# Optimization experiments

Hardware: AMD Instinct MI355X
Metric: run time of the kernel (lower is better)

Reference implementation:

```python
import jax, jax.numpy as jnp
import numpy as np

B, L, D, H, HD = 4, 2048, 1024, 16, 64
SCALE = 1.0 / np.sqrt(HD)
NEG_INF = -1e9


def _apply_rope(x, rope):
    # x: (B, H, L, HD), rope: (L, HD)
    sin = rope[:, ::2]   # (L, HD/2)
    cos = rope[:, 1::2]  # (L, HD/2)
    x_even = x[..., ::2]
    x_odd = x[..., 1::2]
    r_even = x_even * cos - x_odd * sin
    r_odd = x_even * sin + x_odd * cos
    # interleave even/odd back: stack on new last axis then flatten
    return jnp.stack([r_even, r_odd], axis=-1).reshape(x.shape)


def setup_inputs() -> dict:
    key = jax.random.key(0)
    ks = jax.random.split(key, 10)
    s = 0.02
    inp = {
        "q_in": jax.random.normal(ks[0], (B, L, D), jnp.float32),
        "k_in": jax.random.normal(ks[1], (B, L, D), jnp.float32),
        "v_in": jax.random.normal(ks[2], (B, L, D), jnp.float32),
        "mask": jnp.broadcast_to(jnp.tril(jnp.ones((L, L), bool)), (B, L, L)),
        "rope": jax.random.normal(ks[3], (L, HD), jnp.float32),
        "Wq": jax.random.normal(ks[4], (D, H * HD), jnp.float32) * s,
        "bq": jnp.zeros((H * HD,), jnp.float32),
        "Wkv": jax.random.normal(ks[5], (D, 2 * H * HD), jnp.float32) * s,
        "bkv": jnp.zeros((2 * H * HD,), jnp.float32),
        "Wp": jax.random.normal(ks[6], (H * HD, D), jnp.float32) * s,
        "bp": jnp.zeros((D,), jnp.float32),
    }
    return inp


def reference(q_in, k_in, v_in, mask, rope, Wq, bq, Wkv, bkv, Wp, bp):
    q = q_in @ Wq + bq                       # (B, Lq, H*HD)
    kv = k_in @ Wkv + bkv                    # (B, Lk, 2*H*HD)
    k, v = jnp.split(kv, 2, axis=-1)
    q = q.reshape(B, L, H, HD).transpose(0, 2, 1, 3)  # (B, H, Lq, HD)
    k = k.reshape(B, L, H, HD).transpose(0, 2, 1, 3)
    v = v.reshape(B, L, H, HD).transpose(0, 2, 1, 3)
    # rope.shape[0] == Lq == Lk, so both branches fire
    q = _apply_rope(q, rope)
    k = _apply_rope(k, rope)
    logits = jnp.einsum("bhqd,bhkd->bhqk", q, k) * SCALE
    logits = jnp.where(mask[:, None, :, :], logits, NEG_INF)
    attn = jax.nn.softmax(logits, axis=-1)
    out = jnp.einsum("bhqk,bhkd->bhqd", attn, v)
    out = out.transpose(0, 2, 1, 3).reshape(B, L, H * HD)
    return out @ Wp + bp
```

## Files before the change

### kernel.cpp

```cpp
#include <hip/hip_runtime.h>
#include <hip/hip_bf16.h>

typedef __hip_bfloat16 bf16;
typedef short s16x8 __attribute__((ext_vector_type(8)));
typedef float f32x4 __attribute__((ext_vector_type(4)));

#define MFMA16(a, b, c) __builtin_amdgcn_mfma_f32_16x16x32_bf16(a, b, c, 0, 0, 0)
#define SCALE 0.125f

typedef __attribute__((address_space(1))) void gvoid;
typedef __attribute__((address_space(3))) void lvoid;

static __device__ __forceinline__ void lds_cp16(const bf16* g, bf16* l) {
    __builtin_amdgcn_global_load_lds((gvoid*)g, (lvoid*)l, 16, 0, 0);
}

__global__ void cast8_f32(const float* __restrict__ src, bf16* __restrict__ dst,
                          int n) {
    int i = (blockIdx.x * 256 + threadIdx.x) * 8;
    if (i >= n) return;
    float4 a = *(const float4*)(src + i);
    float4 b = *(const float4*)(src + i + 4);
    bf16 o[8];
    o[0] = __float2bfloat16(a.x); o[1] = __float2bfloat16(a.y);
    o[2] = __float2bfloat16(a.z); o[3] = __float2bfloat16(a.w);
    o[4] = __float2bfloat16(b.x); o[5] = __float2bfloat16(b.y);
    o[6] = __float2bfloat16(b.z); o[7] = __float2bfloat16(b.w);
    *(uint4*)(dst + i) = *(const uint4*)o;
}

__global__ void cast8_f32_dual(const float* __restrict__ s0,
                               bf16* __restrict__ d0,
                               const float* __restrict__ s1,
                               bf16* __restrict__ d1, int n) {
    int i = (blockIdx.x * 256 + threadIdx.x) * 8;
    const float* src;
    bf16* dst;
    if (i < n) {
        src = s0; dst = d0;
    } else {
        src = s1; dst = d1; i -= n;
    }
    float4 a = *(const float4*)(src + i);
    float4 b = *(const float4*)(src + i + 4);
    bf16 o[8];
    o[0] = __float2bfloat16(a.x); o[1] = __float2bfloat16(a.y);
    o[2] = __float2bfloat16(a.z); o[3] = __float2bfloat16(a.w);
    o[4] = __float2bfloat16(b.x); o[5] = __float2bfloat16(b.y);
    o[6] = __float2bfloat16(b.z); o[7] = __float2bfloat16(b.w);
    *(uint4*)(dst + i) = *(const uint4*)o;
}

__global__ void cast_biases(const float* __restrict__ bq,
                            const float* __restrict__ bkv,
                            const float* __restrict__ bp,
                            bf16* __restrict__ bqc, bf16* __restrict__ bkvc,
                            bf16* __restrict__ bpc) {
    int i = (blockIdx.x * 256 + threadIdx.x) * 8;
    const float* src;
    bf16* dst;
    int off;
    if (i < 1024) {
        src = bq; dst = bqc; off = i;
    } else if (i < 3072) {
        src = bkv; dst = bkvc; off = i - 1024;
    } else {
        src = bp; dst = bpc; off = i - 3072;
    }
    float4 a = *(const float4*)(src + off);
    float4 b = *(const float4*)(src + off + 4);
    bf16 o[8];
    o[0] = __float2bfloat16(a.x); o[1] = __float2bfloat16(a.y);
    o[2] = __float2bfloat16(a.z); o[3] = __float2bfloat16(a.w);
    o[4] = __float2bfloat16(b.x); o[5] = __float2bfloat16(b.y);
    o[6] = __float2bfloat16(b.z); o[7] = __float2bfloat16(b.w);
    *(uint4*)(dst + off) = *(const uint4*)o;
}

__global__ void transpose_cast3(const float* __restrict__ Wq,
                                bf16* __restrict__ WqT,
                                const float* __restrict__ Wkv,
                                bf16* __restrict__ WkvT,
                                const float* __restrict__ Wp,
                                bf16* __restrict__ WpT) {
    __shared__ bf16 t[32][33];
    const float* in;
    bf16* out;
    int C;
    int bx = blockIdx.x;
    if (bx < 32) {
        in = Wq; out = WqT; C = 1024;
    } else if (bx < 96) {
        in = Wkv; out = WkvT; C = 2048; bx -= 32;
    } else {
        in = Wp; out = WpT; C = 1024; bx -= 96;
    }
    int c0 = bx * 32, r0 = blockIdx.y * 32;
    for (int i = threadIdx.y; i < 32; i += 8)
        t[i][threadIdx.x] =
            __float2bfloat16(in[(size_t)(r0 + i) * C + c0 + threadIdx.x]);
    __syncthreads();
    for (int i = threadIdx.y; i < 32; i += 8)
        out[(size_t)(c0 + i) * 1024 + r0 + threadIdx.x] = t[threadIdx.x][i];
}

template <int EPI, int ROPE>
__device__ __forceinline__ void gemm_core(
    const bf16* __restrict__ A, const bf16* __restrict__ BT,
    const bf16* __restrict__ bias, const bf16* __restrict__ ropetab,
    void* __restrict__ out0, bf16* __restrict__ out1, int N, int K, int bx,
    int by, bf16* smA, bf16* smB) {
    const int tid = threadIdx.x;
    const int lane = tid & 63;
    const int wave = tid >> 6;
    const int lm = lane & 15;
    const int lq = lane >> 4;
    const int bm0 = by * 128;
    const int bn0 = bx * 128;
    const int wm = (wave >> 1) * 64;
    const int wn = (wave & 1) * 64;
    const int x7 = lm & 7;

    int srow[4], scol[4], sdst[4];
#pragma unroll
    for (int j = 0; j < 4; ++j) {
        int o = (wave * 4 + j) * 1024 + lane * 16;
        srow[j] = o >> 7;
        scol[j] = (((o >> 4) & 7) ^ (srow[j] & 7)) * 8;
        sdst[j] = (wave * 4 + j) * 512;
    }

    const f32x4 z4 = {0.f, 0.f, 0.f, 0.f};
    f32x4 acc[4][4];
#pragma unroll
    for (int i = 0; i < 4; ++i)
#pragma unroll
        for (int j = 0; j < 4; ++j) acc[i][j] = z4;

    const bf16* gA = A + (size_t)bm0 * K;
    const bf16* gB = BT + (size_t)bn0 * K;
    const int nk = K >> 6;
    for (int kt = 0; kt < nk; ++kt) {
        const size_t ko = (size_t)kt * 64;
#pragma unroll
        for (int j = 0; j < 4; ++j) {
            lds_cp16(gA + (size_t)srow[j] * K + ko + scol[j], smA + sdst[j]);
            lds_cp16(gB + (size_t)srow[j] * K + ko + scol[j], smB + sdst[j]);
        }
        __syncthreads();

#pragma unroll
        for (int kk = 0; kk < 2; ++kk) {
            s16x8 af[4], bfr[4];
#pragma unroll
            for (int i = 0; i < 4; ++i) {
                const int c16 = kk * 4 + lq;
                af[i] = *(const s16x8*)(smA + (wm + i * 16 + lm) * 64 +
                                        ((c16 ^ x7) * 8));
                bfr[i] = *(const s16x8*)(smB + (wn + i * 16 + lm) * 64 +
                                         ((c16 ^ x7) * 8));
            }
            __builtin_amdgcn_s_setprio(1);
#pragma unroll
            for (int i = 0; i < 4; ++i)
#pragma unroll
                for (int j = 0; j < 4; ++j)
                    acc[i][j] = MFMA16(af[i], bfr[j], acc[i][j]);
            __builtin_amdgcn_s_setprio(0);
        }
        __syncthreads();
    }

#pragma unroll
    for (int j = 0; j < 4; ++j) {
        const int n = bn0 + wn + j * 16 + lm;
        const float bv = __bfloat162float(bias[n]);
#pragma unroll
        for (int i = 0; i < 4; ++i) {
#pragma unroll
            for (int r = 0; r < 4; ++r) {
                const int m = bm0 + wm + i * 16 + lq * 4 + r;
                float v = acc[i][j][r] + bv;
                if (EPI == 0) {
                    ((float*)out0)[(size_t)m * N + n] = v;
                } else {
                    const int b = m >> 11, l = m & 2047;
                    if (EPI == 2 && n >= 1024) {
                        const int n2 = n - 1024;
                        const int h = n2 >> 6, hd = n2 & 63;
                        out1[(((size_t)(b * 16 + h) * 64) + hd) * 2048 + l] =
                            __float2bfloat16(v);
                    } else {
                        if (ROPE) {
                            float w = __shfl_xor(v, 1, 64);
                            unsigned sc = ((const unsigned*)
                                               ropetab)[l * 32 + ((n & 63) >> 1)];
                            float sn = __uint_as_float(sc << 16);
                            float cs = __uint_as_float(sc & 0xffff0000u);
                            v = (n & 1) ? (w * sn + v * cs) : (v * cs - w * sn);
                        }
                        const int h = n >> 6, hd = n & 63;
                        ((bf16*)out0)[(((size_t)(b * 16 + h) * 2048) + l) * 64 +
                                      hd] = __float2bfloat16(v);
                    }
                }
            }
        }
    }
}

__global__ __launch_bounds__(256) void gemm_qk(
    const bf16* __restrict__ qbf, const bf16* __restrict__ WqT,
    const bf16* __restrict__ bqc, const bf16* __restrict__ kbf,
    const bf16* __restrict__ WkvT, const bf16* __restrict__ bkvc,
    const bf16* __restrict__ ropec, bf16* __restrict__ qw,
    bf16* __restrict__ kw, bf16* __restrict__ vtw) {
    __shared__ __align__(16) bf16 smA[128 * 64];
    __shared__ __align__(16) bf16 smB[128 * 64];
    const int lid = blockIdx.x + 24 * blockIdx.y;
    const int xcd = lid & 7;
    const int slot = lid >> 3;
    const int by = xcd * 8 + (slot & 7);
    const int bx = slot >> 3;
    if (bx < 8)
        gemm_core<1, 1>(qbf, WqT, bqc, ropec, qw, (bf16*)nullptr, 1024, 1024,
                        bx, by, smA, smB);
    else
        gemm_core<2, 1>(kbf, WkvT, bkvc, ropec, kw, vtw, 2048, 1024, bx - 8,
                        by, smA, smB);
}

__global__ __launch_bounds__(256) void gemm_out(const bf16* __restrict__ A,
                                                const bf16* __restrict__ WpT,
                                                const bf16* __restrict__ bpc,
                                                float* __restrict__ out) {
    __shared__ __align__(16) bf16 smA[128 * 64];
    __shared__ __align__(16) bf16 smB[128 * 64];
    const int lid = blockIdx.x + 8 * blockIdx.y;
    const int xcd = lid & 7;
    const int slot = lid >> 3;
    const int by = xcd * 8 + (slot & 7);
    const int bx = slot >> 3;
    gemm_core<0, 0>(A, WpT, bpc, (const bf16*)nullptr, out, (bf16*)nullptr,
                    1024, 1024, bx, by, smA, smB);
}

__global__ __launch_bounds__(256, 4) void attn_causal(
    const bf16* __restrict__ Q, const bf16* __restrict__ Kc,
    const bf16* __restrict__ VT, bf16* __restrict__ O) {
    __shared__ __align__(16) bf16 smK[64 * 64];
    __shared__ __align__(16) bf16 smV[64 * 64];
    __shared__ __align__(16) bf16 p_lds[4][2][16 * 40];

    const int tid = threadIdx.x;
    const int lane = tid & 63;
    const int wave = tid >> 6;
    const int lm = lane & 15;
    const int lq = lane >> 4;
    const int x7 = lm & 7;
    const int bh = blockIdx.x;
    const int ya = (int)blockIdx.y >> 2, yb = (int)blockIdx.y & 3;
    const int base4 = (ya == 0) ? 15 : (ya == 1) ? 8 : (ya == 2) ? 7 : 0;
    const int pj = base4 + ((ya & 1) ? yb : -yb);
    const int qblk = pj * 128;
    const int q0 = qblk + wave * 16;
    const int nt = (qblk >> 6) + 2;
    const int b = bh >> 4, h = bh & 15;
    const int q0u = __builtin_amdgcn_readfirstlane(q0);

    const bf16* kp = Kc + (size_t)bh * 2048 * 64;
    const bf16* vp = VT + (size_t)bh * 64 * 2048;
    bf16* plA = &p_lds[wave][0][0];
    bf16* plB = &p_lds[wave][1][0];
    const f32x4 z4 = {0.f, 0.f, 0.f, 0.f};

    int srow[2], scol[2], sdst[2];
#pragma unroll
    for (int j = 0; j < 2; ++j) {
        int o = (wave * 2 + j) * 1024 + lane * 16;
        srow[j] = o >> 7;
        scol[j] = (((o >> 4) & 7) ^ (srow[j] & 7)) * 8;
        sdst[j] = (wave * 2 + j) * 512;
    }

    const bf16* qp = Q + ((size_t)bh * 2048 + q0) * 64;
    s16x8 aq0 = *(const s16x8*)(qp + lm * 64 + lq * 8);
    s16x8 aq1 = *(const s16x8*)(qp + lm * 64 + 32 + lq * 8);
    s16x8 aq2 = *(const s16x8*)(qp + 64 * 64 + lm * 64 + lq * 8);
    s16x8 aq3 = *(const s16x8*)(qp + 64 * 64 + lm * 64 + 32 + lq * 8);

    f32x4 o0[4], o1[4];
#pragma unroll
    for (int c = 0; c < 4; ++c) { o0[c] = z4; o1[c] = z4; }
    float ls0[4] = {0.f, 0.f, 0.f, 0.f};
    float ls1[4] = {0.f, 0.f, 0.f, 0.f};

#define ATTEND_SET(AQ0, AQ1, OO, LS, ROWBASE, ROWU)                           \
    {                                                                         \
        s16x8 kf[8];                                                          \
        _Pragma("unroll") for (int i = 0; i < 8; ++i) {                       \
            const int key = lm + (i >> 1) * 16;                               \
            const int c16 = (i & 1) * 4 + lq;                                 \
            kf[i] = *(const s16x8*)(smK + key * 64 + ((c16 ^ x7) * 8));       \
        }                                                                     \
        __builtin_amdgcn_s_setprio(1);                                        \
        f32x4 sA0 = z4, sA1 = z4, sB0 = z4, sB1 = z4;                         \
        sA0 = MFMA16(AQ0, kf[0], sA0);                                        \
        sA0 = MFMA16(AQ1, kf[1], sA0);                                        \
        sA1 = MFMA16(AQ0, kf[2], sA1);                                        \
        sA1 = MFMA16(AQ1, kf[3], sA1);                                        \
        sB0 = MFMA16(AQ0, kf[4], sB0);                                        \
        sB0 = MFMA16(AQ1, kf[5], sB0);                                        \
        sB1 = MFMA16(AQ0, kf[6], sB1);                                        \
        sB1 = MFMA16(AQ1, kf[7], sB1);                                        \
        __builtin_amdgcn_s_setprio(0);                                        \
        if (kb + 63 <= (ROWU)) {                                              \
            _Pragma("unroll") for (int r = 0; r < 4; ++r) {                   \
                float pA0 = __expf(sA0[r] * SCALE);                           \
                float pA1 = __expf(sA1[r] * SCALE);                           \
                float pB0 = __expf(sB0[r] * SCALE);                           \
                float pB1 = __expf(sB1[r] * SCALE);                           \
                LS[r] += (pA0 + pA1) + (pB0 + pB1);                           \
                plA[(lq * 4 + r) * 40 + lm] = __float2bfloat16(pA0);          \
                plA[(lq * 4 + r) * 40 + 16 + lm] = __float2bfloat16(pA1);     \
                plB[(lq * 4 + r) * 40 + lm] = __float2bfloat16(pB0);          \
                plB[(lq * 4 + r) * 40 + 16 + lm] = __float2bfloat16(pB1);     \
            }                                                                 \
        } else {                                                              \
            _Pragma("unroll") for (int r = 0; r < 4; ++r) {                   \
                const int rowg = (ROWBASE) + lq * 4 + r;                      \
                float pA0 = (kb + lm <= rowg) ? __expf(sA0[r] * SCALE) : 0.f; \
                float pA1 =                                                   \
                    (kb + 16 + lm <= rowg) ? __expf(sA1[r] * SCALE) : 0.f;    \
                float pB0 =                                                   \
                    (kb + 32 + lm <= rowg) ? __expf(sB0[r] * SCALE) : 0.f;    \
                float pB1 =                                                   \
                    (kb + 48 + lm <= rowg) ? __expf(sB1[r] * SCALE) : 0.f;    \
                LS[r] += (pA0 + pA1) + (pB0 + pB1);                           \
                plA[(lq * 4 + r) * 40 + lm] = __float2bfloat16(pA0);          \
                plA[(lq * 4 + r) * 40 + 16 + lm] = __float2bfloat16(pA1);     \
                plB[(lq * 4 + r) * 40 + lm] = __float2bfloat16(pB0);          \
                plB[(lq * 4 + r) * 40 + 16 + lm] = __float2bfloat16(pB1);     \
            }                                                                 \
        }                                                                     \
        s16x8 paA = *(const s16x8*)(plA + lm * 40 + lq * 8);                  \
        s16x8 paB = *(const s16x8*)(plB + lm * 40 + lq * 8);                  \
        __builtin_amdgcn_s_setprio(1);                                        \
        _Pragma("unroll") for (int c = 0; c < 4; ++c) {                       \
            const int hd = c * 16 + lm;                                       \
            s16x8 bvA = *(const s16x8*)(smV + hd * 64 + ((lq ^ x7) * 8));     \
            s16x8 bvB =                                                       \
                *(const s16x8*)(smV + hd * 64 + (((lq + 4) ^ x7) * 8));       \
            OO[c] = MFMA16(paA, bvA, OO[c]);                                  \
            OO[c] = MFMA16(paB, bvB, OO[c]);                                  \
        }                                                                     \
        __builtin_amdgcn_s_setprio(0);                                        \
    }

    for (int it = 0; it < nt; ++it) {
        const int kb = it * 64;
#pragma unroll
        for (int j = 0; j < 2; ++j) {
            lds_cp16(kp + (size_t)(kb + srow[j]) * 64 + scol[j],
                     smK + sdst[j]);
            lds_cp16(vp + (size_t)srow[j] * 2048 + kb + scol[j],
                     smV + sdst[j]);
        }
        __syncthreads();

        if (it < nt - 1) {
            ATTEND_SET(aq0, aq1, o0, ls0, q0, q0u);
        }
        ATTEND_SET(aq2, aq3, o1, ls1, q0 + 64, q0u + 64);

        __syncthreads();
    }
#undef ATTEND_SET

#pragma unroll
    for (int r = 0; r < 4; ++r) {
        float s = ls0[r];
        s += __shfl_xor(s, 1, 64);
        s += __shfl_xor(s, 2, 64);
        s += __shfl_xor(s, 4, 64);
        s += __shfl_xor(s, 8, 64);
        ls0[r] = s;
        float t = ls1[r];
        t += __shfl_xor(t, 1, 64);
        t += __shfl_xor(t, 2, 64);
        t += __shfl_xor(t, 4, 64);
        t += __shfl_xor(t, 8, 64);
        ls1[r] = t;
    }

#pragma unroll
    for (int c = 0; c < 4; ++c) {
#pragma unroll
        for (int r = 0; r < 4; ++r) {
            const int hd = c * 16 + lm;
            const int l0 = q0 + lq * 4 + r;
            O[((size_t)(b * 2048 + l0)) * 1024 + h * 64 + hd] =
                __float2bfloat16(o0[c][r] / ls0[r]);
            const int l1 = l0 + 64;
            O[((size_t)(b * 2048 + l1)) * 1024 + h * 64 + hd] =
                __float2bfloat16(o1[c][r] / ls1[r]);
        }
    }
}

extern "C" void kernel_launch(void* const* d_in, const int* in_sizes, int n_in,
                              void* d_out, int out_size, void* d_ws,
                              size_t ws_size, hipStream_t stream) {
    const float* q_in = (const float*)d_in[0];
    const float* k_in = (const float*)d_in[1];
    const float* rope = (const float*)d_in[4];
    const float* Wq = (const float*)d_in[5];
    const float* bq = (const float*)d_in[6];
    const float* Wkv = (const float*)d_in[7];
    const float* bkv = (const float*)d_in[8];
    const float* Wp = (const float*)d_in[9];
    const float* bp = (const float*)d_in[10];
    float* out = (float*)d_out;

    char* ws = (char*)d_ws;
    bf16* bqc = (bf16*)ws;   ws += 2048;
    bf16* bkvc = (bf16*)ws;  ws += 4096;
    bf16* bpc = (bf16*)ws;   ws += 2048;
    bf16* ropec = (bf16*)ws; ws += 262144;
    bf16* WqT = (bf16*)ws;   ws += 2097152;
    bf16* WkvT = (bf16*)ws;  ws += 4194304;
    bf16* WpT = (bf16*)ws;   ws += 2097152;
    bf16* qw = (bf16*)ws;    ws += 16777216;
    bf16* kw = (bf16*)ws;    ws += 16777216;
    bf16* vtw = (bf16*)ws;   ws += 16777216;
    bf16* aw = (bf16*)ws;    ws += 16777216;
    bf16* qbf = aw;
    bf16* kbf = (bf16*)d_out;

    dim3 blk(256);
    dim3 tb(32, 8);

    cast8_f32<<<64, blk, 0, stream>>>(rope, ropec, 131072);
    cast_biases<<<2, blk, 0, stream>>>(bq, bkv, bp, bqc, bkvc, bpc);
    cast8_f32_dual<<<8192, blk, 0, stream>>>(q_in, qbf, k_in, kbf, 8388608);

    transpose_cast3<<<dim3(128, 32), tb, 0, stream>>>(Wq, WqT, Wkv, WkvT, Wp,
                                                      WpT);

    gemm_qk<<<dim3(24, 64), blk, 0, stream>>>(qbf, WqT, bqc, kbf, WkvT, bkvc,
                                              ropec, qw, kw, vtw);

    attn_causal<<<dim3(64, 16), blk, 0, stream>>>(qw, kw, vtw, aw);

    gemm_out<<<dim3(8, 64), blk, 0, stream>>>(aw, WpT, bpc, out);
}
```

Measured before the change: 210.4 us.

## Merge prep kernels into one launch and stage V-transpose epilogue through LDS

New measurement: 182.8 us, median of 3. 13.1% less time.

```diff
diff --git a/kernel.cpp b/kernel.cpp
--- a/kernel.cpp
+++ b/kernel.cpp
@@ -15,10 +15,8 @@
     __builtin_amdgcn_global_load_lds((gvoid*)g, (lvoid*)l, 16, 0, 0);
 }
 
-__global__ void cast8_f32(const float* __restrict__ src, bf16* __restrict__ dst,
-                          int n) {
-    int i = (blockIdx.x * 256 + threadIdx.x) * 8;
-    if (i >= n) return;
+static __device__ __forceinline__ void cast8(const float* __restrict__ src,
+                                             bf16* __restrict__ dst, int i) {
     float4 a = *(const float4*)(src + i);
     float4 b = *(const float4*)(src + i + 4);
     bf16 o[8];
@@ -29,79 +27,67 @@
     *(uint4*)(dst + i) = *(const uint4*)o;
 }
 
-__global__ void cast8_f32_dual(const float* __restrict__ s0,
-                               bf16* __restrict__ d0,
-                               const float* __restrict__ s1,
-                               bf16* __restrict__ d1, int n) {
-    int i = (blockIdx.x * 256 + threadIdx.x) * 8;
-    const float* src;
-    bf16* dst;
-    if (i < n) {
-        src = s0; dst = d0;
+__global__ __launch_bounds__(256) void prep(
+    const float* __restrict__ q_in, bf16* __restrict__ qbf,
+    const float* __restrict__ k_in, bf16* __restrict__ kbf,
+    const float* __restrict__ rope, bf16* __restrict__ ropec,
+    const float* __restrict__ bq, const float* __restrict__ bkv,
+    const float* __restrict__ bp, bf16* __restrict__ bqc,
+    bf16* __restrict__ bkvc, bf16* __restrict__ bpc,
+    const float* __restrict__ Wq, bf16* __restrict__ WqT,
+    const float* __restrict__ Wkv, bf16* __restrict__ WkvT,
+    const float* __restrict__ Wp, bf16* __restrict__ WpT) {
+    __shared__ bf16 t[32][33];
+    const int blk = blockIdx.x;
+    const int tid = threadIdx.x;
+    if (blk < 8192) {
+        int i = (blk * 256 + tid) * 8;
+        const float* src;
+        bf16* dst;
+        if (i < 8388608) {
+            src = q_in; dst = qbf;
+        } else {
+            src = k_in; dst = kbf; i -= 8388608;
+        }
+        cast8(src, dst, i);
+    } else if (blk < 12288) {
+        int t2 = blk - 8192;
+        int bx = t2 & 127;
+        const int y = t2 >> 7;
+        const float* in;
+        bf16* out;
+        int C;
+        if (bx < 32) {
+            in = Wq; out = WqT; C = 1024;
+        } else if (bx < 96) {
+            in = Wkv; out = WkvT; C = 2048; bx -= 32;
+        } else {
+            in = Wp; out = WpT; C = 1024; bx -= 96;
+        }
+        const int tx = tid & 31, ty = tid >> 5;
+        const int c0 = bx * 32, r0 = y * 32;
+        for (int i = ty; i < 32; i += 8)
+            t[i][tx] = __float2bfloat16(in[(size_t)(r0 + i) * C + c0 + tx]);
+        __syncthreads();
+        for (int i = ty; i < 32; i += 8)
+            out[(size_t)(c0 + i) * 1024 + r0 + tx] = t[tx][i];
+    } else if (blk < 12352) {
+        int i = ((blk - 12288) * 256 + tid) * 8;
+        cast8(rope, ropec, i);
     } else {
-        src = s1; dst = d1; i -= n;
-    }
-    float4 a = *(const float4*)(src + i);
-    float4 b = *(const float4*)(src + i + 4);
-    bf16 o[8];
-    o[0] = __float2bfloat16(a.x); o[1] = __float2bfloat16(a.y);
-    o[2] = __float2bfloat16(a.z); o[3] = __float2bfloat16(a.w);
-    o[4] = __float2bfloat16(b.x); o[5] = __float2bfloat16(b.y);
-    o[6] = __float2bfloat16(b.z); o[7] = __float2bfloat16(b.w);
-    *(uint4*)(dst + i) = *(const uint4*)o;
-}
-
-__global__ void cast_biases(const float* __restrict__ bq,
-                            const float* __restrict__ bkv,
-                            const float* __restrict__ bp,
-                            bf16* __restrict__ bqc, bf16* __restrict__ bkvc,
-                            bf16* __restrict__ bpc) {
-    int i = (blockIdx.x * 256 + threadIdx.x) * 8;
-    const float* src;
-    bf16* dst;
-    int off;
-    if (i < 1024) {
-        src = bq; dst = bqc; off = i;
-    } else if (i < 3072) {
-        src = bkv; dst = bkvc; off = i - 1024;
-    } else {
-        src = bp; dst = bpc; off = i - 3072;
-    }
-    float4 a = *(const float4*)(src + off);
-    float4 b = *(const float4*)(src + off + 4);
-    bf16 o[8];
-    o[0] = __float2bfloat16(a.x); o[1] = __float2bfloat16(a.y);
-    o[2] = __float2bfloat16(a.z); o[3] = __float2bfloat16(a.w);
-    o[4] = __float2bfloat16(b.x); o[5] = __float2bfloat16(b.y);
-    o[6] = __float2bfloat16(b.z); o[7] = __float2bfloat16(b.w);
-    *(uint4*)(dst + off) = *(const uint4*)o;
-}
-
-__global__ void transpose_cast3(const float* __restrict__ Wq,
-                                bf16* __restrict__ WqT,
-                                const float* __restrict__ Wkv,
-                                bf16* __restrict__ WkvT,
-                                const float* __restrict__ Wp,
-                                bf16* __restrict__ WpT) {
-    __shared__ bf16 t[32][33];
-    const float* in;
-    bf16* out;
-    int C;
-    int bx = blockIdx.x;
-    if (bx < 32) {
-        in = Wq; out = WqT; C = 1024;
-    } else if (bx < 96) {
-        in = Wkv; out = WkvT; C = 2048; bx -= 32;
-    } else {
-        in = Wp; out = WpT; C = 1024; bx -= 96;
-    }
-    int c0 = bx * 32, r0 = blockIdx.y * 32;
-    for (int i = threadIdx.y; i < 32; i += 8)
-        t[i][threadIdx.x] =
-            __float2bfloat16(in[(size_t)(r0 + i) * C + c0 + threadIdx.x]);
-    __syncthreads();
-    for (int i = threadIdx.y; i < 32; i += 8)
-        out[(size_t)(c0 + i) * 1024 + r0 + threadIdx.x] = t[threadIdx.x][i];
+        int i = ((blk - 12352) * 256 + tid) * 8;
+        const float* src;
+        bf16* dst;
+        int off;
+        if (i < 1024) {
+            src = bq; dst = bqc; off = i;
+        } else if (i < 3072) {
+            src = bkv; dst = bkvc; off = i - 1024;
+        } else {
+            src = bp; dst = bpc; off = i - 3072;
+        }
+        cast8(src, dst, off);
+    }
 }
 
 template <int EPI, int ROPE>
@@ -171,6 +157,41 @@
         __syncthreads();
     }
 
+    if (EPI == 2 && bn0 >= 1024) {
+        bf16* T = smA;
+#pragma unroll
+        for (int j = 0; j < 4; ++j) {
+            const int nl = wn + j * 16 + lm;
+            const float bv = __bfloat162float(bias[bn0 + nl]);
+            const int xsw = (nl & 7) << 3;
+#pragma unroll
+            for (int i = 0; i < 4; ++i) {
+                const int m0 = wm + i * 16 + lq * 4;
+                bf16 pk[4];
+#pragma unroll
+                for (int r = 0; r < 4; ++r)
+                    pk[r] = __float2bfloat16(acc[i][j][r] + bv);
+                *(uint2*)(T + nl * 128 + (m0 ^ xsw)) = *(const uint2*)pk;
+            }
+        }
+        __syncthreads();
+        const int b = bm0 >> 11;
+        const int lbase = bm0 & 2047;
+#pragma unroll
+        for (int p = 0; p < 8; ++p) {
+            const int task = p * 256 + tid;
+            const int row = task >> 4;
+            const int chunk = task & 15;
+            const int m8 = chunk * 8;
+            uint4 v = *(const uint4*)(T + row * 128 + (m8 ^ ((row & 7) << 3)));
+            const int n2 = bn0 - 1024 + row;
+            const int h = n2 >> 6, hd = n2 & 63;
+            *(uint4*)(out1 + (((size_t)(b * 16 + h) * 64) + hd) * 2048 +
+                      lbase + m8) = v;
+        }
+        return;
+    }
+
 #pragma unroll
     for (int j = 0; j < 4; ++j) {
         const int n = bn0 + wn + j * 16 + lm;
@@ -185,24 +206,17 @@
                     ((float*)out0)[(size_t)m * N + n] = v;
                 } else {
                     const int b = m >> 11, l = m & 2047;
-                    if (EPI == 2 && n >= 1024) {
-                        const int n2 = n - 1024;
-                        const int h = n2 >> 6, hd = n2 & 63;
-                        out1[(((size_t)(b * 16 + h) * 64) + hd) * 2048 + l] =
-                            __float2bfloat16(v);
-                    } else {
-                        if (ROPE) {
-                            float w = __shfl_xor(v, 1, 64);
-                            unsigned sc = ((const unsigned*)
-                                               ropetab)[l * 32 + ((n & 63) >> 1)];
-                            float sn = __uint_as_float(sc << 16);
-                            float cs = __uint_as_float(sc & 0xffff0000u);
-                            v = (n & 1) ? (w * sn + v * cs) : (v * cs - w * sn);
-                        }
-                        const int h = n >> 6, hd = n & 63;
-                        ((bf16*)out0)[(((size_t)(b * 16 + h) * 2048) + l) * 64 +
-                                      hd] = __float2bfloat16(v);
+                    if (ROPE) {
+                        float w = __shfl_xor(v, 1, 64);
+                        unsigned sc =
+                            ((const unsigned*)ropetab)[l * 32 + ((n & 63) >> 1)];
+                        float sn = __uint_as_float(sc << 16);
+                        float cs = __uint_as_float(sc & 0xffff0000u);
+                        v = (n & 1) ? (w * sn + v * cs) : (v * cs - w * sn);
                     }
+                    const int h = (n & 1023) >> 6, hd = n & 63;
+                    ((bf16*)out0)[(((size_t)(b * 16 + h) * 2048) + l) * 64 +
+                                  hd] = __float2bfloat16(v);
                 }
             }
         }
@@ -215,8 +229,7 @@
     const bf16* __restrict__ WkvT, const bf16* __restrict__ bkvc,
     const bf16* __restrict__ ropec, bf16* __restrict__ qw,
     bf16* __restrict__ kw, bf16* __restrict__ vtw) {
-    __shared__ __align__(16) bf16 smA[128 * 64];
-    __shared__ __align__(16) bf16 smB[128 * 64];
+    __shared__ __align__(16) bf16 sm[2 * 128 * 64];
     const int lid = blockIdx.x + 24 * blockIdx.y;
     const int xcd = lid & 7;
     const int slot = lid >> 3;
@@ -224,25 +237,24 @@
     const int bx = slot >> 3;
     if (bx < 8)
         gemm_core<1, 1>(qbf, WqT, bqc, ropec, qw, (bf16*)nullptr, 1024, 1024,
-                        bx, by, smA, smB);
+                        bx, by, sm, sm + 8192);
     else
         gemm_core<2, 1>(kbf, WkvT, bkvc, ropec, kw, vtw, 2048, 1024, bx - 8,
-                        by, smA, smB);
+                        by, sm, sm + 8192);
 }
 
 __global__ __launch_bounds__(256) void gemm_out(const bf16* __restrict__ A,
                                                 const bf16* __restrict__ WpT,
                                                 const bf16* __restrict__ bpc,
                                                 float* __restrict__ out) {
-    __shared__ __align__(16) bf16 smA[128 * 64];
-    __shared__ __align__(16) bf16 smB[128 * 64];
+    __shared__ __align__(16) bf16 sm[2 * 128 * 64];
     const int lid = blockIdx.x + 8 * blockIdx.y;
     const int xcd = lid & 7;
     const int slot = lid >> 3;
     const int by = xcd * 8 + (slot & 7);
     const int bx = slot >> 3;
     gemm_core<0, 0>(A, WpT, bpc, (const bf16*)nullptr, out, (bf16*)nullptr,
-                    1024, 1024, bx, by, smA, smB);
+                    1024, 1024, bx, by, sm, sm + 8192);
 }
 
 __global__ __launch_bounds__(256, 4) void attn_causal(
@@ -438,14 +450,10 @@
     bf16* kbf = (bf16*)d_out;
 
     dim3 blk(256);
-    dim3 tb(32, 8);
-
-    cast8_f32<<<64, blk, 0, stream>>>(rope, ropec, 131072);
-    cast_biases<<<2, blk, 0, stream>>>(bq, bkv, bp, bqc, bkvc, bpc);
-    cast8_f32_dual<<<8192, blk, 0, stream>>>(q_in, qbf, k_in, kbf, 8388608);
-
-    transpose_cast3<<<dim3(128, 32), tb, 0, stream>>>(Wq, WqT, Wkv, WkvT, Wp,
-                                                      WpT);
+
+    prep<<<12354, blk, 0, stream>>>(q_in, qbf, k_in, kbf, rope, ropec, bq, bkv,
+                                    bp, bqc, bkvc, bpc, Wq, WqT, Wkv, WkvT, Wp,
+                                    WpT);
 
     gemm_qk<<<dim3(24, 64), blk, 0, stream>>>(qbf, WqT, bqc, kbf, WkvT, bkvc,
                                               ropec, qw, kw, vtw);
```
